# Optimization experiments

Measured on AMD Instinct MI355X. Metric: run time of the kernel, lower is better.

## Reference

```python
import jax, jax.numpy as jnp
import numpy as np

EMBED_DIM = 64       # embedding_dim (latent channels)
NUM_ATOMS = 1024     # num_embeddings (dictionary atoms)
SPARSITY = 8         # sparsity_level
N_PIXELS = 16384     # flattened latent pixels (e.g. B=16, 32x32 grid)
DIAG_EPS = 1e-4
CHOL_EPS = 1e-6


def setup_inputs() -> dict:
    key = jax.random.key(0)
    kx, kd = jax.random.split(key)
    X = jax.random.normal(kx, (EMBED_DIM, N_PIXELS), dtype=jnp.float32)
    # dictionary parameter initialized as randn * 0.02, per the module __init__
    D = jax.random.normal(kd, (EMBED_DIM, NUM_ATOMS), dtype=jnp.float32) * 0.02
    return {"X": X, "D": D}


def _nan0(x):
    return jnp.nan_to_num(x, nan=0.0, posinf=0.0, neginf=0.0)


def _batched_omp(X, D, sparsity_level):
    """Batched OMP with sequential Cholesky updates.

    X: [d, N] signals, D: [d, K] dictionary.
    Returns (I [N, S] int32 support indices, coeffs [N, S] ordered coefficients).
    """
    X = _nan0(X)
    D = _nan0(D)
    d, n = X.shape
    k = D.shape[1]
    rows = jnp.arange(n)

    G = D.T @ D + DIAG_EPS * jnp.eye(k, dtype=D.dtype)   # [K, K] Gram
    h_bar = (D.T @ X).T                                   # [N, K] correlations
    h = h_bar
    mask = jnp.zeros((n, k), dtype=bool)                  # selected-atom mask
    L = None                                              # batched Cholesky [N, s, s]
    I = jnp.zeros((n, 0), dtype=jnp.int32)
    coeffs = jnp.zeros((n, 0), dtype=X.dtype)

    for s in range(sparsity_level):  # static unroll, S is small
        scores = jnp.where(mask, jnp.asarray(-1.0, X.dtype), jnp.abs(h))
        idx = jnp.argmax(scores, axis=1)                  # [N]
        mask = mask.at[rows, idx].set(True)
        diag_g = G[idx, idx][:, None, None]               # [N, 1, 1]
        if s == 0:
            L = jnp.sqrt(jnp.clip(diag_g, CHOL_EPS))      # [N, 1, 1]
        else:
            # G[I[n, j], idx[n]] for each batch element n -> [N, s, 1]
            G_col = G[I, idx[:, None]][..., None]
            w = jax.scipy.linalg.solve_triangular(L, G_col, lower=True)  # [N, s, 1]
            wt = jnp.swapaxes(w, 1, 2)                                   # [N, 1, s]
            corner = jnp.sqrt(jnp.clip(diag_g - jnp.sum(w * w, axis=1, keepdims=True), CHOL_EPS))
            zeros_col = jnp.zeros((n, s, 1), dtype=X.dtype)
            L = jnp.concatenate(
                [jnp.concatenate([L, zeros_col], axis=2),
                 jnp.concatenate([wt, corner], axis=2)], axis=1)          # [N, s+1, s+1]
        I = jnp.concatenate([I, idx[:, None].astype(jnp.int32)], axis=1)  # [N, s+1]
        # solve (L L^T) x = h_bar[support] via two triangular solves (cholesky_solve)
        h_stack = jnp.take_along_axis(h_bar, I, axis=1)[..., None]        # [N, s+1, 1]
        y = jax.scipy.linalg.solve_triangular(L, h_stack, lower=True)
        x_stack = jax.scipy.linalg.solve_triangular(jnp.swapaxes(L, 1, 2), y, lower=False)
        coeffs = _nan0(x_stack[..., 0])                                   # [N, s+1]
        # beta = coeffs @ G[support, :]  -> residual correlation update
        beta = jnp.einsum('ns,nsk->nk', coeffs, G[I])
        h = _nan0(h_bar - beta)
    return I, coeffs


def reference(X, D):
    I, coeffs = _batched_omp(X, D, SPARSITY)
    atoms = D[:, I]                                  # [d, N, S]
    recon = jnp.einsum('ns,dns->nd', coeffs, atoms)  # [N, d] sparse reconstruction
    return recon, I, coeffs
```

## Files before the change

kernel.cpp:

```cpp
#include <hip/hip_runtime.h>
#include <cmath>

#define NPIX 16384
#define NATOM 1024
#define DIM 64
#define SPAR 8

__global__ __launch_bounds__(256) void k_pre(const float* __restrict__ X,
                                             const float* __restrict__ D,
                                             float* __restrict__ G,
                                             float* __restrict__ Dt,
                                             float* __restrict__ Gd,
                                             float* __restrict__ HB) {
  __shared__ float smem[2 * DIM * 128];
  const int b = blockIdx.x;
  if (b < 256) {
    const int i0 = (b >> 4) * 64, j0 = (b & 15) * 64;
    float(*sA)[65] = (float(*)[65])smem;
    float(*sB)[65] = (float(*)[65])(smem + DIM * 65);
    for (int t = threadIdx.x; t < DIM * 16; t += 256) {
      int d = t >> 4, c4 = (t & 15) * 4;
      *reinterpret_cast<float4*>(&sA[d][c4]) =
          *reinterpret_cast<const float4*>(&D[(size_t)d * NATOM + i0 + c4]);
      *reinterpret_cast<float4*>(&sB[d][c4]) =
          *reinterpret_cast<const float4*>(&D[(size_t)d * NATOM + j0 + c4]);
    }
    __syncthreads();
    const int ty = (threadIdx.x >> 4) * 4;
    const int tx = (threadIdx.x & 15) * 4;
    double acc[4][4];
#pragma unroll
    for (int ii = 0; ii < 4; ++ii)
#pragma unroll
      for (int jj = 0; jj < 4; ++jj) acc[ii][jj] = 0.0;
    for (int d = 0; d < DIM; ++d) {
      float a[4], bb[4];
#pragma unroll
      for (int ii = 0; ii < 4; ++ii) a[ii] = sA[d][ty + ii];
#pragma unroll
      for (int jj = 0; jj < 4; ++jj) bb[jj] = sB[d][tx + jj];
#pragma unroll
      for (int ii = 0; ii < 4; ++ii)
#pragma unroll
        for (int jj = 0; jj < 4; ++jj)
          acc[ii][jj] += (double)a[ii] * (double)bb[jj];
    }
#pragma unroll
    for (int ii = 0; ii < 4; ++ii)
#pragma unroll
      for (int jj = 0; jj < 4; ++jj) {
        const int k1 = i0 + ty + ii, k2 = j0 + tx + jj;
        float g = (float)acc[ii][jj];
        if (k1 == k2) {
          g += 1e-4f;
          Gd[k1] = g;
        }
        G[(size_t)k1 * NATOM + k2] = g;
      }
  } else if (b < 320) {
    const int base = (b - 256) * 1024 + threadIdx.x * 4;
    float4 v = *reinterpret_cast<const float4*>(&D[base]);
    const float vv[4] = {v.x, v.y, v.z, v.w};
#pragma unroll
    for (int e = 0; e < 4; ++e) {
      int idx = base + e;
      Dt[(size_t)(idx & (NATOM - 1)) * DIM + (idx >> 10)] = vv[e];
    }
  } else {
    const int bx = b - 320;
    const int n0 = (bx & 127) * 128, k0 = (bx >> 7) * 128;
    float(*sX)[128] = (float(*)[128])smem;
    float(*sD)[128] = (float(*)[128])(smem + DIM * 128);
    for (int i = threadIdx.x; i < DIM * 32; i += 256) {
      int d = i >> 5, c4 = (i & 31) * 4;
      *reinterpret_cast<float4*>(&sX[d][c4]) =
          *reinterpret_cast<const float4*>(&X[(size_t)d * NPIX + n0 + c4]);
      *reinterpret_cast<float4*>(&sD[d][c4]) =
          *reinterpret_cast<const float4*>(&D[(size_t)d * NATOM + k0 + c4]);
    }
    __syncthreads();
    const int nl = (threadIdx.x & 15) * 8;
    const int kl = (threadIdx.x >> 4) * 8;
    float acc[8][8];
#pragma unroll
    for (int i = 0; i < 8; ++i)
#pragma unroll
      for (int j = 0; j < 8; ++j) acc[i][j] = 0.f;
#pragma unroll 4
    for (int d = 0; d < DIM; ++d) {
      float xv[8], dv[8];
      *reinterpret_cast<float4*>(&xv[0]) = *reinterpret_cast<float4*>(&sX[d][nl]);
      *reinterpret_cast<float4*>(&xv[4]) = *reinterpret_cast<float4*>(&sX[d][nl + 4]);
      *reinterpret_cast<float4*>(&dv[0]) = *reinterpret_cast<float4*>(&sD[d][kl]);
      *reinterpret_cast<float4*>(&dv[4]) = *reinterpret_cast<float4*>(&sD[d][kl + 4]);
#pragma unroll
      for (int i = 0; i < 8; ++i)
#pragma unroll
        for (int j = 0; j < 8; ++j) acc[i][j] = fmaf(xv[i], dv[j], acc[i][j]);
    }
#pragma unroll
    for (int i = 0; i < 8; ++i)
#pragma unroll
      for (int j = 0; j < 2; ++j)
        *reinterpret_cast<float4*>(
            &HB[(size_t)(n0 + nl + i) * NATOM + k0 + kl + j * 4]) =
            *reinterpret_cast<float4*>(&acc[i][j * 4]);
  }
}

template <int CTRL>
__device__ __forceinline__ float dpp_fmax(float x) {
  int s = __builtin_amdgcn_update_dpp(__float_as_int(x), __float_as_int(x),
                                      CTRL, 0xf, 0xf, false);
  return fmaxf(x, __int_as_float(s));
}
__device__ __forceinline__ float wave_max_bcast(float x) {
  x = dpp_fmax<0x111>(x);
  x = dpp_fmax<0x112>(x);
  x = dpp_fmax<0x114>(x);
  x = dpp_fmax<0x118>(x);
  x = dpp_fmax<0x142>(x);
  x = dpp_fmax<0x143>(x);
  return __int_as_float(__builtin_amdgcn_readlane(__float_as_int(x), 63));
}

__global__ __launch_bounds__(128, 3) void k_omp2(const float* __restrict__ HB,
                                                 const float* __restrict__ Dt,
                                                 const float* __restrict__ G,
                                                 const float* __restrict__ Gd,
                                                 float* __restrict__ out) {
  const int lane = threadIdx.x & 63;
  const int wave = threadIdx.x >> 6;
  const int kbase = wave * 512 + lane * 8;
  const int n = __builtin_amdgcn_readfirstlane(blockIdx.x);

  __shared__ float sM[2][2];
  __shared__ int sC[2][2];
  __shared__ float sCoef[SPAR];

  float hb[8];
#pragma unroll
  for (int q = 0; q < 2; ++q) {
    float4 v = *reinterpret_cast<const float4*>(
        &HB[(size_t)n * NATOM + kbase + q * 4]);
    hb[q * 4 + 0] = v.x; hb[q * 4 + 1] = v.y;
    hb[q * 4 + 2] = v.z; hb[q * 4 + 3] = v.w;
  }
#pragma unroll
  for (int j = 0; j < 8; ++j) asm volatile("" : "+v"(hb[j]));

  int selI[SPAR];
  float rows[SPAR - 1][8];
  float Lm[SPAR][SPAR], invL[SPAR], ysel[SPAR], coefF[SPAR];

#pragma unroll 8
  for (int s = 0; s < SPAR; ++s) {
    float h[8];
#pragma unroll
    for (int j = 0; j < 8; ++j) {
      float hv = hb[j];
#pragma unroll
      for (int i = 0; i < SPAR - 1; ++i)
        if (i < s) hv = fmaf(-coefF[i], rows[i][j], hv);
      h[j] = hv;
    }
    float ml = fmaxf(fmaxf(fmaxf(fabsf(h[0]), fabsf(h[1])), fabsf(h[2])), fabsf(h[3]));
    float mh = fmaxf(fmaxf(fmaxf(fabsf(h[4]), fabsf(h[5])), fabsf(h[6])), fabsf(h[7]));
    const float Mw = wave_max_bcast(fmaxf(ml, mh));
    unsigned cand = NATOM;
#pragma unroll
    for (int j = 7; j >= 0; --j)
      cand = (fabsf(h[j]) == Mw) ? (unsigned)(kbase + j) : cand;
    unsigned long long bal = __ballot(cand != (unsigned)NATOM);
    const int fl = __ffsll(bal) - 1;
    const int cw = __builtin_amdgcn_readlane((int)cand, fl);
    if (lane == 0) {
      sM[s & 1][wave] = Mw;
      sC[s & 1][wave] = cw;
    }
    __syncthreads();
    const float M0 = sM[s & 1][0], M1 = sM[s & 1][1];
    const int c0 = sC[s & 1][0], c1 = sC[s & 1][1];
    int bkv;
    if (M0 > M1) bkv = c0;
    else if (M1 > M0) bkv = c1;
    else bkv = c0 < c1 ? c0 : c1;
    const int bk = __builtin_amdgcn_readfirstlane(bkv);
    selI[s] = bk;

    if ((bk >> 9) == wave && lane == ((bk >> 3) & 63)) {
#pragma unroll
      for (int j = 0; j < 8; ++j)
        if (j == (bk & 7)) hb[j] = __builtin_nanf("");
    }

    if (s < SPAR - 1) {
#pragma unroll
      for (int q = 0; q < 2; ++q) {
        float4 rv = *reinterpret_cast<const float4*>(
            &G[(size_t)bk * NATOM + kbase + q * 4]);
        rows[s][q * 4 + 0] = rv.x; rows[s][q * 4 + 1] = rv.y;
        rows[s][q * 4 + 2] = rv.z; rows[s][q * 4 + 3] = rv.w;
      }
    }

    if (wave == 1) {
      const float hbs = HB[(size_t)n * NATOM + bk];
      const float diag = Gd[bk];
      float w[SPAR];
      float sq = 0.f;
#pragma unroll
      for (int i = 0; i < SPAR; ++i)
        if (i < s) {
          float a = G[(size_t)selI[i] * NATOM + bk];
#pragma unroll
          for (int t = 0; t < SPAR; ++t)
            if (t < i) a = fmaf(-Lm[i][t], w[t], a);
          w[i] = a * invL[i];
          sq += w[i] * w[i];
          Lm[s][i] = w[i];
        }
      float cc = diag - sq;
      if (cc < 1e-6f) cc = 1e-6f;
      invL[s] = 1.0f / sqrtf(cc);

      {
        float a = hbs;
#pragma unroll
        for (int t = 0; t < SPAR; ++t)
          if (t < s) a = fmaf(-Lm[s][t], ysel[t], a);
        ysel[s] = a * invL[s];
      }
#pragma unroll
      for (int i = SPAR - 1; i >= 0; --i)
        if (i <= s) {
          float a = ysel[i];
#pragma unroll
          for (int t = 0; t < SPAR; ++t)
            if (t > i && t <= s) a = fmaf(-Lm[t][i], coefF[t], a);
          coefF[i] = a * invL[i];
        }
      if (lane == 0) {
#pragma unroll
        for (int i = 0; i < SPAR; ++i)
          if (i <= s) sCoef[i] = coefF[i];
      }
    }
    __syncthreads();
    if (wave == 0) {
#pragma unroll
      for (int i = 0; i < SPAR; ++i)
        if (i <= s) coefF[i] = sCoef[i];
    }

    if (s < SPAR - 1) {
#pragma unroll
      for (int j = 0; j < 8; ++j) asm volatile("" : "+v"(rows[s][j]));
    }
  }

  if (wave == 0) {
    double r = 0.0;
#pragma unroll
    for (int i = 0; i < SPAR; ++i)
      r += (double)coefF[i] * (double)Dt[(size_t)selI[i] * DIM + lane];
    out[(size_t)n * DIM + lane] = (float)r;
  } else {
    float fi = 0.f, fc = 0.f;
#pragma unroll
    for (int i = 0; i < SPAR; ++i)
      if (lane == i) { fi = (float)selI[i]; fc = coefF[i]; }
    if (lane < SPAR) {
      out[(size_t)NPIX * DIM + (size_t)n * SPAR + lane] = fi;
      out[(size_t)NPIX * DIM + (size_t)NPIX * SPAR + (size_t)n * SPAR + lane] = fc;
    }
  }
}

__global__ __launch_bounds__(64) void k_omp_fb(const float* __restrict__ X,
                                               const float* __restrict__ D,
                                               const float* __restrict__ G,
                                               const float* __restrict__ Gd,
                                               float* __restrict__ out) {
  const int lane = threadIdx.x & 63;
  const int lane16 = lane * 16;
  const int n = __builtin_amdgcn_readfirstlane(blockIdx.x);

  float hb[16];
  {
    double a[16];
#pragma unroll
    for (int j = 0; j < 16; ++j) a[j] = 0.0;
    for (int d = 0; d < DIM; ++d) {
      float xd = X[(size_t)d * NPIX + n];
#pragma unroll
      for (int j = 0; j < 16; ++j)
        a[j] += (double)xd * (double)D[(size_t)d * NATOM + lane16 + j];
    }
#pragma unroll
    for (int j = 0; j < 16; ++j) hb[j] = (float)a[j];
  }
#pragma unroll
  for (int j = 0; j < 16; ++j) asm volatile("" : "+v"(hb[j]));

  int selI[SPAR];
  float rows[SPAR - 1][16];
  float Lm[SPAR][SPAR], invL[SPAR], ysel[SPAR], coefF[SPAR];

#pragma unroll 8
  for (int s = 0; s < SPAR; ++s) {
    float h[16];
#pragma unroll
    for (int j = 0; j < 16; ++j) {
      float hv = hb[j];
#pragma unroll
      for (int i = 0; i < SPAR - 1; ++i)
        if (i < s) hv = fmaf(-coefF[i], rows[i][j], hv);
      h[j] = hv;
    }
    float m0 = fmaxf(fmaxf(fmaxf(fabsf(h[0]), fabsf(h[1])), fabsf(h[2])), fabsf(h[3]));
    float m1 = fmaxf(fmaxf(fmaxf(fabsf(h[4]), fabsf(h[5])), fabsf(h[6])), fabsf(h[7]));
    float m2 = fmaxf(fmaxf(fmaxf(fabsf(h[8]), fabsf(h[9])), fabsf(h[10])), fabsf(h[11]));
    float m3 = fmaxf(fmaxf(fmaxf(fabsf(h[12]), fabsf(h[13])), fabsf(h[14])), fabsf(h[15]));
    const float M = wave_max_bcast(fmaxf(fmaxf(m0, m1), fmaxf(m2, m3)));
    unsigned cand = NATOM;
#pragma unroll
    for (int j = 15; j >= 0; --j)
      cand = (fabsf(h[j]) == M) ? (unsigned)(lane16 + j) : cand;
    unsigned long long bal = __ballot(cand != (unsigned)NATOM);
    const int fl = __ffsll(bal) - 1;
    const int bk = __builtin_amdgcn_readlane((int)cand, fl);
    selI[s] = bk;
    const int bl = bk >> 4, bj = bk & 15;

    float v = 0.f;
#pragma unroll
    for (int j = 0; j < 16; ++j)
      if (j == bj) v = hb[j];
    const float hbs =
        __int_as_float(__builtin_amdgcn_readlane(__float_as_int(v), bl));

#pragma unroll
    for (int j = 0; j < 16; ++j)
      if (j == bj && lane == bl) hb[j] = __builtin_nanf("");

    if (s < SPAR - 1) {
#pragma unroll
      for (int q = 0; q < 4; ++q) {
        float4 rv = *reinterpret_cast<const float4*>(
            &G[(size_t)bk * NATOM + lane16 + q * 4]);
        rows[s][q * 4 + 0] = rv.x; rows[s][q * 4 + 1] = rv.y;
        rows[s][q * 4 + 2] = rv.z; rows[s][q * 4 + 3] = rv.w;
      }
    }

    const float diag = Gd[bk];
    float w[SPAR];
    float sq = 0.f;
#pragma unroll
    for (int i = 0; i < SPAR; ++i)
      if (i < s) {
        float a = G[(size_t)selI[i] * NATOM + bk];
#pragma unroll
        for (int t = 0; t < SPAR; ++t)
          if (t < i) a = fmaf(-Lm[i][t], w[t], a);
        w[i] = a * invL[i];
        sq += w[i] * w[i];
        Lm[s][i] = w[i];
      }
    float cc = diag - sq;
    if (cc < 1e-6f) cc = 1e-6f;
    invL[s] = 1.0f / sqrtf(cc);
    {
      float a = hbs;
#pragma unroll
      for (int t = 0; t < SPAR; ++t)
        if (t < s) a = fmaf(-Lm[s][t], ysel[t], a);
      ysel[s] = a * invL[s];
    }
#pragma unroll
    for (int i = SPAR - 1; i >= 0; --i)
      if (i <= s) {
        float a = ysel[i];
#pragma unroll
        for (int t = 0; t < SPAR; ++t)
          if (t > i && t <= s) a = fmaf(-Lm[t][i], coefF[t], a);
        coefF[i] = a * invL[i];
      }
    if (s < SPAR - 1) {
#pragma unroll
      for (int j = 0; j < 16; ++j) asm volatile("" : "+v"(rows[s][j]));
    }
  }

  double r = 0.0;
#pragma unroll
  for (int i = 0; i < SPAR; ++i)
    r += (double)coefF[i] * (double)D[(size_t)lane * NATOM + selI[i]];
  out[(size_t)n * DIM + lane] = (float)r;

  float fi = 0.f, fc = 0.f;
#pragma unroll
  for (int i = 0; i < SPAR; ++i)
    if (lane == i) { fi = (float)selI[i]; fc = coefF[i]; }
  if (lane < SPAR) {
    out[(size_t)NPIX * DIM + (size_t)n * SPAR + lane] = fi;
    out[(size_t)NPIX * DIM + (size_t)NPIX * SPAR + (size_t)n * SPAR + lane] = fc;
  }
}

__global__ __launch_bounds__(256) void k_gram(const float* __restrict__ D,
                                              float* __restrict__ G,
                                              float* __restrict__ Gd) {
  int k1 = blockIdx.x;
  __shared__ float d1[DIM];
  if (threadIdx.x < DIM) d1[threadIdx.x] = D[(size_t)threadIdx.x * NATOM + k1];
  __syncthreads();
  for (int k2 = threadIdx.x; k2 < NATOM; k2 += 256) {
    double acc = 0.0;
#pragma unroll
    for (int d = 0; d < DIM; ++d)
      acc += (double)d1[d] * (double)D[(size_t)d * NATOM + k2];
    float g = (float)acc;
    if (k2 == k1) {
      g += 1e-4f;
      Gd[k1] = g;
    }
    G[(size_t)k1 * NATOM + k2] = g;
  }
}

extern "C" void kernel_launch(void* const* d_in, const int* in_sizes, int n_in,
                              void* d_out, int out_size, void* d_ws,
                              size_t ws_size, hipStream_t stream) {
  const float* X = (const float*)d_in[0];
  const float* D = (const float*)d_in[1];
  float* out = (float*)d_out;
  float* G = (float*)d_ws;
  float* Dt = G + (size_t)NATOM * NATOM;
  float* Gd = Dt + (size_t)NATOM * DIM;
  float* HB = Gd + NATOM;
  const size_t needFull =
      ((size_t)NATOM * NATOM + (size_t)NATOM * DIM + NATOM +
       (size_t)NPIX * NATOM) * sizeof(float);

  if (ws_size >= needFull) {
    k_pre<<<dim3(1344), dim3(256), 0, stream>>>(X, D, G, Dt, Gd, HB);
    k_omp2<<<dim3(NPIX), dim3(128), 0, stream>>>(HB, Dt, G, Gd, out);
  } else {
    k_gram<<<dim3(NATOM), dim3(256), 0, stream>>>(D, G, Gd);
    k_omp_fb<<<dim3(NPIX), dim3(64), 0, stream>>>(X, D, G, Gd, out);
  }
}
```

Baseline: 110.6 us.

## Split per-pixel OMP across four waves and rotate the serial solver wave

The per-pixel OMP kernel now runs 256 threads (four waves) instead of 128, so each lane holds 4 correlation entries instead of 8, and the argmax merge combines four wave maxima. The wave that runs the serial Cholesky update and solve rotates with the pixel index, spreading that scalar-heavy work across SIMDs instead of always using wave 1. The goal is more parallelism and fewer registers per lane for the residual update and max reduction. The cost is more block-wide synchronisation, a larger cross-wave merge, and three of four waves idling during the serial solve.

```diff
diff --git a/kernel.cpp b/kernel.cpp
--- a/kernel.cpp
+++ b/kernel.cpp
@@ -124,52 +124,49 @@
   return __int_as_float(__builtin_amdgcn_readlane(__float_as_int(x), 63));
 }
 
-__global__ __launch_bounds__(128, 3) void k_omp2(const float* __restrict__ HB,
+__global__ __launch_bounds__(256, 4) void k_omp4(const float* __restrict__ HB,
                                                  const float* __restrict__ Dt,
                                                  const float* __restrict__ G,
                                                  const float* __restrict__ Gd,
                                                  float* __restrict__ out) {
   const int lane = threadIdx.x & 63;
   const int wave = threadIdx.x >> 6;
-  const int kbase = wave * 512 + lane * 8;
+  const int kbase = wave * 256 + lane * 4;
   const int n = __builtin_amdgcn_readfirstlane(blockIdx.x);
-
-  __shared__ float sM[2][2];
-  __shared__ int sC[2][2];
+  const int sv = n & 3;
+
+  __shared__ float sM[2][4];
+  __shared__ int sC[2][4];
   __shared__ float sCoef[SPAR];
 
-  float hb[8];
-#pragma unroll
-  for (int q = 0; q < 2; ++q) {
-    float4 v = *reinterpret_cast<const float4*>(
-        &HB[(size_t)n * NATOM + kbase + q * 4]);
-    hb[q * 4 + 0] = v.x; hb[q * 4 + 1] = v.y;
-    hb[q * 4 + 2] = v.z; hb[q * 4 + 3] = v.w;
-  }
-#pragma unroll
-  for (int j = 0; j < 8; ++j) asm volatile("" : "+v"(hb[j]));
+  float hb[4];
+  {
+    float4 v = *reinterpret_cast<const float4*>(&HB[(size_t)n * NATOM + kbase]);
+    hb[0] = v.x; hb[1] = v.y; hb[2] = v.z; hb[3] = v.w;
+  }
+#pragma unroll
+  for (int j = 0; j < 4; ++j) asm volatile("" : "+v"(hb[j]));
 
   int selI[SPAR];
-  float rows[SPAR - 1][8];
+  float rows[SPAR - 1][4];
   float Lm[SPAR][SPAR], invL[SPAR], ysel[SPAR], coefF[SPAR];
 
 #pragma unroll 8
   for (int s = 0; s < SPAR; ++s) {
-    float h[8];
-#pragma unroll
-    for (int j = 0; j < 8; ++j) {
+    float h[4];
+#pragma unroll
+    for (int j = 0; j < 4; ++j) {
       float hv = hb[j];
 #pragma unroll
       for (int i = 0; i < SPAR - 1; ++i)
         if (i < s) hv = fmaf(-coefF[i], rows[i][j], hv);
       h[j] = hv;
     }
-    float ml = fmaxf(fmaxf(fmaxf(fabsf(h[0]), fabsf(h[1])), fabsf(h[2])), fabsf(h[3]));
-    float mh = fmaxf(fmaxf(fmaxf(fabsf(h[4]), fabsf(h[5])), fabsf(h[6])), fabsf(h[7]));
-    const float Mw = wave_max_bcast(fmaxf(ml, mh));
+    const float Mw = wave_max_bcast(
+        fmaxf(fmaxf(fabsf(h[0]), fabsf(h[1])), fmaxf(fabsf(h[2]), fabsf(h[3]))));
     unsigned cand = NATOM;
 #pragma unroll
-    for (int j = 7; j >= 0; --j)
+    for (int j = 3; j >= 0; --j)
       cand = (fabsf(h[j]) == Mw) ? (unsigned)(kbase + j) : cand;
     unsigned long long bal = __ballot(cand != (unsigned)NATOM);
     const int fl = __ffsll(bal) - 1;
@@ -179,32 +176,34 @@
       sC[s & 1][wave] = cw;
     }
     __syncthreads();
-    const float M0 = sM[s & 1][0], M1 = sM[s & 1][1];
-    const int c0 = sC[s & 1][0], c1 = sC[s & 1][1];
-    int bkv;
-    if (M0 > M1) bkv = c0;
-    else if (M1 > M0) bkv = c1;
-    else bkv = c0 < c1 ? c0 : c1;
+    const float Ma = sM[s & 1][0], Mb = sM[s & 1][1];
+    const float Mc = sM[s & 1][2], Md = sM[s & 1][3];
+    const float Ms = fmaxf(fmaxf(Ma, Mb), fmaxf(Mc, Md));
+    int bkv = NATOM;
+    {
+      int c;
+      c = (Ma == Ms) ? sC[s & 1][0] : NATOM; bkv = c < bkv ? c : bkv;
+      c = (Mb == Ms) ? sC[s & 1][1] : NATOM; bkv = c < bkv ? c : bkv;
+      c = (Mc == Ms) ? sC[s & 1][2] : NATOM; bkv = c < bkv ? c : bkv;
+      c = (Md == Ms) ? sC[s & 1][3] : NATOM; bkv = c < bkv ? c : bkv;
+    }
     const int bk = __builtin_amdgcn_readfirstlane(bkv);
     selI[s] = bk;
 
-    if ((bk >> 9) == wave && lane == ((bk >> 3) & 63)) {
-#pragma unroll
-      for (int j = 0; j < 8; ++j)
-        if (j == (bk & 7)) hb[j] = __builtin_nanf("");
+    if ((bk >> 8) == wave && lane == ((bk >> 2) & 63)) {
+#pragma unroll
+      for (int j = 0; j < 4; ++j)
+        if (j == (bk & 3)) hb[j] = __builtin_nanf("");
     }
 
     if (s < SPAR - 1) {
-#pragma unroll
-      for (int q = 0; q < 2; ++q) {
-        float4 rv = *reinterpret_cast<const float4*>(
-            &G[(size_t)bk * NATOM + kbase + q * 4]);
-        rows[s][q * 4 + 0] = rv.x; rows[s][q * 4 + 1] = rv.y;
-        rows[s][q * 4 + 2] = rv.z; rows[s][q * 4 + 3] = rv.w;
-      }
-    }
-
-    if (wave == 1) {
+      float4 rv = *reinterpret_cast<const float4*>(
+          &G[(size_t)bk * NATOM + kbase]);
+      rows[s][0] = rv.x; rows[s][1] = rv.y;
+      rows[s][2] = rv.z; rows[s][3] = rv.w;
+    }
+
+    if (wave == sv) {
       const float hbs = HB[(size_t)n * NATOM + bk];
       const float diag = Gd[bk];
       float w[SPAR];
@@ -247,7 +246,7 @@
       }
     }
     __syncthreads();
-    if (wave == 0) {
+    if (wave != sv) {
 #pragma unroll
       for (int i = 0; i < SPAR; ++i)
         if (i <= s) coefF[i] = sCoef[i];
@@ -255,17 +254,17 @@
 
     if (s < SPAR - 1) {
 #pragma unroll
-      for (int j = 0; j < 8; ++j) asm volatile("" : "+v"(rows[s][j]));
-    }
-  }
-
-  if (wave == 0) {
+      for (int j = 0; j < 4; ++j) asm volatile("" : "+v"(rows[s][j]));
+    }
+  }
+
+  if (wave == ((sv + 1) & 3)) {
     double r = 0.0;
 #pragma unroll
     for (int i = 0; i < SPAR; ++i)
       r += (double)coefF[i] * (double)Dt[(size_t)selI[i] * DIM + lane];
     out[(size_t)n * DIM + lane] = (float)r;
-  } else {
+  } else if (wave == ((sv + 2) & 3)) {
     float fi = 0.f, fc = 0.f;
 #pragma unroll
     for (int i = 0; i < SPAR; ++i)
@@ -446,7 +445,7 @@
 
   if (ws_size >= needFull) {
     k_pre<<<dim3(1344), dim3(256), 0, stream>>>(X, D, G, Dt, Gd, HB);
-    k_omp2<<<dim3(NPIX), dim3(128), 0, stream>>>(HB, Dt, G, Gd, out);
+    k_omp4<<<dim3(NPIX), dim3(256), 0, stream>>>(HB, Dt, G, Gd, out);
   } else {
     k_gram<<<dim3(NATOM), dim3(256), 0, stream>>>(D, G, Gd);
     k_omp_fb<<<dim3(NPIX), dim3(64), 0, stream>>>(X, D, G, Gd, out);
```

Result: slower. 139.2 us (+25.8%).
